# Performance work log

Measured on AMD Instinct MI355X. Metric: run time of the kernel, lower is better.

## Reference

```python
import jax, jax.numpy as jnp
import numpy as np

N = 7          # num nodes == conv1 in_channels (PyG: x=None -> node indices, in_channels=num_nodes)
H = 16         # hidden channels (hardcoded in the module)
R = 64         # num_relations
C = 8          # out_channels
E = 8_000_000  # num edges


def setup_inputs() -> dict:
    key = jax.random.key(0)
    ks = jax.random.split(key, 7)
    return dict(
        x=jax.random.normal(ks[0], (N, N), jnp.float32),  # ignored: forward passes None to conv1
        edge_index=jax.random.randint(ks[1], (2, E), 0, N, dtype=jnp.int32),
        edge_type=jax.random.randint(ks[2], (E,), 0, R, dtype=jnp.int32),
        W1=jax.random.normal(ks[3], (R, N, H), jnp.float32) / np.sqrt(N).astype(np.float32),
        root1=jax.random.normal(ks[4], (N, H), jnp.float32) / np.sqrt(N).astype(np.float32),
        b1=jnp.zeros((H,), jnp.float32),
        W2=jax.random.normal(ks[5], (R, H, C), jnp.float32) / np.sqrt(H).astype(np.float32),
        root2=jax.random.normal(ks[6], (H, C), jnp.float32) / np.sqrt(H).astype(np.float32),
        b2=jnp.zeros((C,), jnp.float32),
    )


def _rel_mean_norm(dst, edge_type):
    # FastRGCNConv aggr='mean': 1 / max(#in-edges of dst with the same relation, 1), per edge.
    comb = dst * R + edge_type                                    # [E] combined (node, rel) id
    counts = jax.ops.segment_sum(jnp.ones_like(comb, jnp.float32), comb,
                                 num_segments=N * R)              # [N*R]
    return 1.0 / jnp.maximum(counts[comb], 1.0)                   # [E]


def reference(x, edge_index, edge_type, W1, root1, b1, W2, root2, b2):
    src, dst = edge_index[0], edge_index[1]
    norm = _rel_mean_norm(dst, edge_type)                         # [E]

    # layer 1: x is None -> message = W1[edge_type, src] (embedding per relation);
    # root weight acts as an embedding root1[arange(N)] = root1.
    msg1 = W1[edge_type, src] * norm[:, None]                     # [E,H]
    h = jax.ops.segment_sum(msg1, dst, num_segments=N) + root1 + b1
    h = jax.nn.relu(h)                                            # [N,H]

    # layer 2: compute all per-(node, relation) transforms once (N is tiny),
    # then gather per edge — same math as per-edge bmm, avoids [E,H,C] temp.
    hr = jnp.einsum('nh,rhc->nrc', h, W2)                         # [N,R,C]
    msg2 = hr[src, edge_type] * norm[:, None]                     # [E,C]
    out = jax.ops.segment_sum(msg2, dst, num_segments=N) + h @ root2 + b2
    return jax.nn.log_softmax(out, axis=1)                        # [N,C]
```

## Files before the change

kernel.cpp:

```cpp
#include <hip/hip_runtime.h>
#include <hip/hip_bf16.h>

#define NN 7
#define HH 16
#define RR 64
#define CC 8
#define NBINS (NN * RR * NN)

#define HIST_BLOCK 1024
#define HIST_GRID  256
#define NT (HIST_GRID * HIST_BLOCK)
#define NSLOT 8

__global__ __launch_bounds__(HIST_BLOCK) void rgcn_hist(
    const int* __restrict__ src, const int* __restrict__ dst,
    const int* __restrict__ et, int E, int* __restrict__ part) {
    __shared__ int bins[NBINS];
    for (int i = threadIdx.x; i < NBINS; i += HIST_BLOCK) bins[i] = 0;
    __syncthreads();

    const int tid = blockIdx.x * HIST_BLOCK + threadIdx.x;
    const int E4 = E >> 2;
    const int4* s4 = reinterpret_cast<const int4*>(src);
    const int4* d4 = reinterpret_cast<const int4*>(dst);
    const int4* t4 = reinterpret_cast<const int4*>(et);

    if (E4 > 0) {
        for (int base = tid; base < E4; base += NSLOT * NT) {
            int4 S[4], D[4], T[4];
#pragma unroll
            for (int k = 0; k < 4; ++k) {
                int idx = base + k * NT;
                int cl = idx < E4 ? idx : (E4 - 1);
                S[k] = s4[cl]; D[k] = d4[cl]; T[k] = t4[cl];
            }
#pragma unroll
            for (int k = 0; k < NSLOT; ++k) {
                const int slot = k & 3;
                const int add = (base + k * NT < E4) ? 1 : 0;
                atomicAdd(&bins[D[slot].x * (RR * NN) + T[slot].x * NN + S[slot].x], add);
                atomicAdd(&bins[D[slot].y * (RR * NN) + T[slot].y * NN + S[slot].y], add);
                atomicAdd(&bins[D[slot].z * (RR * NN) + T[slot].z * NN + S[slot].z], add);
                atomicAdd(&bins[D[slot].w * (RR * NN) + T[slot].w * NN + S[slot].w], add);
                if (k < NSLOT - 4) {
                    int idx = base + (k + 4) * NT;
                    int cl = idx < E4 ? idx : (E4 - 1);
                    S[slot] = s4[cl]; D[slot] = d4[cl]; T[slot] = t4[cl];
                }
            }
        }
    }
    for (int e = (E4 << 2) + tid; e < E; e += NT) {
        atomicAdd(&bins[dst[e] * (RR * NN) + et[e] * NN + src[e]], 1);
    }

    __syncthreads();
    int4* slice4 = reinterpret_cast<int4*>(part + blockIdx.x * NBINS);
    const int4* bins4 = reinterpret_cast<const int4*>(bins);
    for (int i2 = threadIdx.x; i2 < NBINS / 4; i2 += HIST_BLOCK)
        slice4[i2] = bins4[i2];
}

__global__ __launch_bounds__(256) void rgcn_reduce(
    const int* __restrict__ part, int* __restrict__ gbins) {
    __shared__ int acc[4][64];
    const int lane = threadIdx.x & 63;
    const int chunk = threadIdx.x >> 6;
    const int bin = blockIdx.x * 64 + lane;

    int s = 0;
    const int p0 = chunk * (HIST_GRID / 4);
#pragma unroll 8
    for (int k = 0; k < HIST_GRID / 4; ++k)
        s += part[(p0 + k) * NBINS + bin];
    acc[chunk][lane] = s;
    __syncthreads();
    if (chunk == 0)
        gbins[bin] = acc[0][lane] + acc[1][lane] + acc[2][lane] + acc[3][lane];
}

__global__ __launch_bounds__(1024) void rgcn_finish(
    const int* __restrict__ gbins,
    const float* __restrict__ W1,
    const float* __restrict__ root1,
    const float* __restrict__ b1,
    const float* __restrict__ W2,
    const float* __restrict__ root2,
    const float* __restrict__ b2,
    float* __restrict__ out) {
    __shared__ float cntf[NN][RR][NN];
    __shared__ float w1s[RR * NN * HH];
    __shared__ float w2s[RR * HH * CC];
    __shared__ float p1[NN][HH][4];
    __shared__ float h[NN][HH];
    __shared__ float hr[NN][RR][CC];
    __shared__ float p2[NN][CC][8];
    __shared__ float o[NN][CC];

    const int t = threadIdx.x;
    const int BD = 1024;
    const float4* W1v = reinterpret_cast<const float4*>(W1);
    for (int i = t; i < RR * NN * HH / 4; i += BD)
        reinterpret_cast<float4*>(w1s)[i] = W1v[i];
    const float4* W2v = reinterpret_cast<const float4*>(W2);
    for (int i = t; i < RR * HH * CC / 4; i += BD)
        reinterpret_cast<float4*>(w2s)[i] = W2v[i];
    for (int i = t; i < NN * RR; i += BD) {
        int n = i / RR, r = i % RR;
        const int* gb = gbins + n * (RR * NN) + r * NN;
        int c[NN];
        int tot = 0;
#pragma unroll
        for (int s = 0; s < NN; ++s) { c[s] = gb[s]; tot += c[s]; }
        float inv = 1.0f / (float)(tot > 0 ? tot : 1);
#pragma unroll
        for (int s = 0; s < NN; ++s) cntf[n][r][s] = (float)c[s] * inv;
    }
    __syncthreads();

    for (int i = t; i < NN * HH * 4; i += BD) {
        int n = i >> 6;
        int j = (i >> 2) & (HH - 1);
        int q = i & 3;
        float acc = 0.0f;
        for (int r = q * 16; r < q * 16 + 16; ++r)
            for (int s = 0; s < NN; ++s)
                acc = fmaf(cntf[n][r][s], w1s[(r * NN + s) * HH + j], acc);
        p1[n][j][q] = acc;
    }
    __syncthreads();
    for (int i = t; i < NN * HH; i += BD) {
        int n = i / HH, j = i % HH;
        float acc = root1[n * HH + j] + b1[j] +
                    p1[n][j][0] + p1[n][j][1] + p1[n][j][2] + p1[n][j][3];
        h[n][j] = fmaxf(acc, 0.0f);
    }
    __syncthreads();

    for (int i = t; i < NN * RR * CC; i += BD) {
        int s = i / (RR * CC);
        int rem = i % (RR * CC);
        int r = rem / CC, c = rem % CC;
        float acc = 0.0f;
        for (int j = 0; j < HH; ++j)
            acc = fmaf(h[s][j], w2s[(r * HH + j) * CC + c], acc);
        hr[s][r][c] = acc;
    }
    __syncthreads();

    for (int i = t; i < NN * CC * 8; i += BD) {
        int n = i >> 6;
        int c = (i >> 3) & (CC - 1);
        int q = i & 7;
        float acc = 0.0f;
        for (int r = q * 8; r < q * 8 + 8; ++r)
            for (int s = 0; s < NN; ++s)
                acc = fmaf(cntf[n][r][s], hr[s][r][c], acc);
        if (q == 0) {
            for (int j = 0; j < HH; ++j)
                acc = fmaf(h[n][j], root2[j * CC + c], acc);
            acc += b2[c];
        }
        p2[n][c][q] = acc;
    }
    __syncthreads();
    for (int i = t; i < NN * CC; i += BD) {
        int n = i / CC, c = i % CC;
        float acc = 0.0f;
        for (int q = 0; q < 8; ++q) acc += p2[n][c][q];
        o[n][c] = acc;
    }
    __syncthreads();

    if (t < NN) {
        float m = -1e30f;
        for (int c = 0; c < CC; ++c) m = fmaxf(m, o[t][c]);
        float sum = 0.0f;
        for (int c = 0; c < CC; ++c) sum += __expf(o[t][c] - m);
        float lse = m + __logf(sum);
        for (int c = 0; c < CC; ++c) out[t * CC + c] = o[t][c] - lse;
    }
}

extern "C" void kernel_launch(void* const* d_in, const int* in_sizes, int n_in,
                              void* d_out, int out_size, void* d_ws, size_t ws_size,
                              hipStream_t stream) {
    const int* edge_index = (const int*)d_in[1];
    const int* edge_type  = (const int*)d_in[2];
    const float* W1    = (const float*)d_in[3];
    const float* root1 = (const float*)d_in[4];
    const float* b1    = (const float*)d_in[5];
    const float* W2    = (const float*)d_in[6];
    const float* root2 = (const float*)d_in[7];
    const float* b2    = (const float*)d_in[8];
    float* out = (float*)d_out;

    const int E = in_sizes[2];
    const int* src = edge_index;
    const int* dst = edge_index + E;

    int* part  = (int*)d_ws;
    int* gbins = part + HIST_GRID * NBINS;

    rgcn_hist<<<HIST_GRID, HIST_BLOCK, 0, stream>>>(src, dst, edge_type, E, part);
    rgcn_reduce<<<49, 256, 0, stream>>>(part, gbins);
    rgcn_finish<<<1, 1024, 0, stream>>>(gbins, W1, root1, b1, W2, root2, b2, out);
}
```

Baseline: 37.56 us.

## Fuse histogram reduction and finish into one kernel with atomic counter handoff

Merges the reduce and finish kernels into a single launch. Blocks 1..49 reduce the partial histograms and bump a global counter, while block 0 prefetches the weights into shared memory and spin-waits on that counter before computing the output. The counter is reset by the histogram kernel. This removes one kernel launch and lets the weight loads overlap the reduction. The cost is a spin-wait whose forward progress relies on all blocks being co-resident.

```diff
diff --git a/kernel.cpp b/kernel.cpp
--- a/kernel.cpp
+++ b/kernel.cpp
@@ -12,10 +12,15 @@
 #define NT (HIST_GRID * HIST_BLOCK)
 #define NSLOT 8
 
+#define RED_GRID 50
+
 __global__ __launch_bounds__(HIST_BLOCK) void rgcn_hist(
     const int* __restrict__ src, const int* __restrict__ dst,
-    const int* __restrict__ et, int E, int* __restrict__ part) {
+    const int* __restrict__ et, int E, int* __restrict__ part,
+    int* __restrict__ ctrl) {
     __shared__ int bins[NBINS];
+    if (blockIdx.x == 0 && threadIdx.x == 0)
+        __hip_atomic_store(&ctrl[0], 0, __ATOMIC_RELAXED, __HIP_MEMORY_SCOPE_AGENT);
     for (int i = threadIdx.x; i < NBINS; i += HIST_BLOCK) bins[i] = 0;
     __syncthreads();
 
@@ -61,26 +66,9 @@
         slice4[i2] = bins4[i2];
 }
 
-__global__ __launch_bounds__(256) void rgcn_reduce(
-    const int* __restrict__ part, int* __restrict__ gbins) {
-    __shared__ int acc[4][64];
-    const int lane = threadIdx.x & 63;
-    const int chunk = threadIdx.x >> 6;
-    const int bin = blockIdx.x * 64 + lane;
-
-    int s = 0;
-    const int p0 = chunk * (HIST_GRID / 4);
-#pragma unroll 8
-    for (int k = 0; k < HIST_GRID / 4; ++k)
-        s += part[(p0 + k) * NBINS + bin];
-    acc[chunk][lane] = s;
-    __syncthreads();
-    if (chunk == 0)
-        gbins[bin] = acc[0][lane] + acc[1][lane] + acc[2][lane] + acc[3][lane];
-}
-
-__global__ __launch_bounds__(1024) void rgcn_finish(
-    const int* __restrict__ gbins,
+__global__ __launch_bounds__(1024) void rgcn_redfin(
+    const int* __restrict__ part, int* __restrict__ gbins,
+    int* __restrict__ ctrl,
     const float* __restrict__ W1,
     const float* __restrict__ root1,
     const float* __restrict__ b1,
@@ -88,9 +76,10 @@
     const float* __restrict__ root2,
     const float* __restrict__ b2,
     float* __restrict__ out) {
-    __shared__ float cntf[NN][RR][NN];
     __shared__ float w1s[RR * NN * HH];
     __shared__ float w2s[RR * HH * CC];
+    __shared__ int   redacc[16][64];
+    __shared__ float cntf[NN][RR][NN];
     __shared__ float p1[NN][HH][4];
     __shared__ float h[NN][HH];
     __shared__ float hr[NN][RR][CC];
@@ -98,13 +87,48 @@
     __shared__ float o[NN][CC];
 
     const int t = threadIdx.x;
+    const int b = blockIdx.x;
     const int BD = 1024;
+
+    if (b != 0) {
+        const int binl = t & 63;
+        const int chunk = t >> 6;
+        const int gbin = (b - 1) * 64 + binl;
+        int s = 0;
+#pragma unroll
+        for (int k = 0; k < 16; ++k)
+            s += part[(chunk * 16 + k) * NBINS + gbin];
+        redacc[chunk][binl] = s;
+        __syncthreads();
+        if (t < 64) {
+            int tot = 0;
+#pragma unroll
+            for (int c = 0; c < 16; ++c) tot += redacc[c][t];
+            gbins[(b - 1) * 64 + t] = tot;
+        }
+        __threadfence();
+        __syncthreads();
+        if (t == 0)
+            __hip_atomic_fetch_add(&ctrl[0], 1, __ATOMIC_ACQ_REL,
+                                   __HIP_MEMORY_SCOPE_AGENT);
+        return;
+    }
+
     const float4* W1v = reinterpret_cast<const float4*>(W1);
     for (int i = t; i < RR * NN * HH / 4; i += BD)
         reinterpret_cast<float4*>(w1s)[i] = W1v[i];
     const float4* W2v = reinterpret_cast<const float4*>(W2);
     for (int i = t; i < RR * HH * CC / 4; i += BD)
         reinterpret_cast<float4*>(w2s)[i] = W2v[i];
+
+    if (t == 0) {
+        while (__hip_atomic_load(&ctrl[0], __ATOMIC_ACQUIRE,
+                                 __HIP_MEMORY_SCOPE_AGENT) < RED_GRID - 1)
+            __builtin_amdgcn_s_sleep(2);
+    }
+    __syncthreads();
+    __threadfence();
+
     for (int i = t; i < NN * RR; i += BD) {
         int n = i / RR, r = i % RR;
         const int* gb = gbins + n * (RR * NN) + r * NN;
@@ -201,8 +225,11 @@
 
     int* part  = (int*)d_ws;
     int* gbins = part + HIST_GRID * NBINS;
-
-    rgcn_hist<<<HIST_GRID, HIST_BLOCK, 0, stream>>>(src, dst, edge_type, E, part);
-    rgcn_reduce<<<49, 256, 0, stream>>>(part, gbins);
-    rgcn_finish<<<1, 1024, 0, stream>>>(gbins, W1, root1, b1, W2, root2, b2, out);
+    int* ctrl  = gbins + NBINS;
+
+    rgcn_hist<<<HIST_GRID, HIST_BLOCK, 0, stream>>>(src, dst, edge_type, E,
+                                                    part, ctrl);
+    rgcn_redfin<<<RED_GRID, 1024, 0, stream>>>(part, gbins, ctrl,
+                                               W1, root1, b1, W2, root2, b2,
+                                               out);
 }
```

Measured after the change: 50.81 us. 35.3% more time.
